# Performance work log

Hardware: AMD Instinct MI355X
Metric: run time of the kernel (lower is better)

The kernel has to match this reference:

```python
import jax, jax.numpy as jnp
import numpy as np

DIM = 8      # channels (from CxWxW_Attention(8, 4, False))
HEADS = 4    # num_heads
EPS = 1e-12  # torch F.normalize eps


def setup_inputs() -> dict:
    key = jax.random.key(0)
    k0, k1, k2, k3 = jax.random.split(key, 4)
    b, c, h, w = 16, DIM, 512, 512
    x = jax.random.normal(k0, (b, c, h, w), jnp.float32)
    # 1x1 conv producing qkv (bias=False): weight (3c, c)
    w_qkv = jax.random.normal(k1, (3 * c, c), jnp.float32) * 0.1
    # 3x3 depthwise conv on qkv, groups=3c: weight (3c, 1, 3, 3)
    w_dw = jax.random.normal(k2, (3 * c, 1, 3, 3), jnp.float32) * 0.1
    # 1x1 projection out: weight (c, c)
    w_out = jax.random.normal(k3, (c, c), jnp.float32) * 0.1
    # per-head learned temperature, init ones; broadcasts over (b, head, c, w, w)
    temperature = jnp.ones((HEADS, 1, 1, 1), jnp.float32)
    return dict(x=x, w_qkv=w_qkv, w_dw=w_dw, w_out=w_out, temperature=temperature)


def _dwconv3x3(x, wgt):
    # depthwise 3x3, padding=1, groups = channels
    C = x.shape[1]
    return jax.lax.conv_general_dilated(
        x, wgt, window_strides=(1, 1), padding=((1, 1), (1, 1)),
        dimension_numbers=("NCHW", "OIHW", "NCHW"), feature_group_count=C)


def _l2norm(t):
    # torch.nn.functional.normalize along last dim
    n = jnp.sqrt(jnp.sum(t * t, axis=-1, keepdims=True))
    return t / jnp.maximum(n, EPS)


def reference(x, w_qkv, w_dw, w_out, temperature):
    b, c, h, w = x.shape
    heads, ch = HEADS, c // HEADS
    # qkv = dwconv3x3(conv1x1(x))
    qkv = jnp.einsum("bchw,oc->bohw", x, w_qkv)
    qkv = _dwconv3x3(qkv, w_dw)
    q, k, v = jnp.split(qkv, 3, axis=1)
    # rearrange 'b (head ch) h w -> b head ch w h' : width attends, height = feature
    def split_heads(t):
        return t.reshape(b, heads, ch, h, w).transpose(0, 1, 2, 4, 3)
    q, k, v = split_heads(q), split_heads(k), split_heads(v)
    q = _l2norm(q)
    k = _l2norm(k)
    # attention map of shape (b, head, ch, W, W)  -> the 'C x W x W' attention
    attn = jnp.einsum("bncwh,bncvh->bncwv", q, k) * temperature
    attn = jax.nn.softmax(attn, axis=-1)
    out = jnp.einsum("bncwv,bncvh->bncwh", attn, v)  # (b, head, ch, w, h)
    # rearrange back 'b head ch w h -> b (head ch) h w'
    out = out.transpose(0, 1, 2, 4, 3).reshape(b, c, h, w)
    return jnp.einsum("bchw,oc->bohw", out, w_out)
```

## Files before the change

kernel.cpp:

```cpp
#include <hip/hip_runtime.h>
#include <hip/hip_bf16.h>

typedef __attribute__((ext_vector_type(4))) float f32x4;
typedef __attribute__((ext_vector_type(2))) float f32x2;
typedef __attribute__((ext_vector_type(8))) short s16x8;
typedef __attribute__((ext_vector_type(4))) short s16x4;
typedef __attribute__((ext_vector_type(4))) unsigned short u16x4;

#define HW 512
#define NSLICE 128

union B4 { s16x4 v; __hip_bfloat16 e[4]; };

__global__ __launch_bounds__(256) void qkv_fused(
    const float* __restrict__ x, const float* __restrict__ wqkv,
    const float* __restrict__ wdw,
    __hip_bfloat16* __restrict__ qT, __hip_bfloat16* __restrict__ kT,
    __hip_bfloat16* __restrict__ vS,
    float* __restrict__ qss, float* __restrict__ kss)
{
  const int b = blockIdx.y;
  const int tile = blockIdx.x;
  const int h0 = (tile >> 4) * 32;
  const int w0 = (tile & 15) * 32;
  const int tid = threadIdx.x;

  __shared__ float ts[4][1156][2];
  __shared__ float colsq[4][8][32];
  __shared__ float wq_s[24][8];
  __shared__ float wd_s[24][12];

  if (tid < 192) wq_s[tid >> 3][tid & 7] = wqkv[tid];
  if (tid < 216) wd_s[tid / 9][tid % 9] = wdw[tid];

  float xr[5][8];
  #pragma unroll
  for (int p = 0; p < 5; ++p) {
    int i = tid + p * 256;
    if (i < 1156) {
      int ih = h0 - 1 + i / 34, iw = w0 - 1 + i % 34;
      bool ok = (ih >= 0 && ih < HW && iw >= 0 && iw < HW);
      #pragma unroll
      for (int c = 0; c < 8; ++c)
        xr[p][c] = ok ? x[((size_t)(b * 8 + c) * HW + ih) * HW + iw] : 0.f;
    }
  }
  __syncthreads();

  const int tw = tid & 31;
  const int th = tid >> 5;
  const int lane = tid & 63;
  const int wv = tid >> 6;

  #pragma unroll
  for (int g = 0; g < 3; ++g) {
    #pragma unroll
    for (int p = 0; p < 5; ++p) {
      int i = tid + p * 256;
      if (i < 1156) {
        #pragma unroll
        for (int op = 0; op < 4; ++op) {
          const int o = g * 8 + op * 2;
          float a0 = 0.f, a1 = 0.f;
          #pragma unroll
          for (int c = 0; c < 8; ++c) {
            a0 += xr[p][c] * wq_s[o][c];
            a1 += xr[p][c] * wq_s[o + 1][c];
          }
          ts[op][i][0] = a0;
          ts[op][i][1] = a1;
        }
      }
    }
    __syncthreads();

    #pragma unroll
    for (int op = 0; op < 4; ++op) {
      const int o = g * 8 + op * 2;
      float w2[6][3][2];
      #pragma unroll
      for (int r = 0; r < 6; ++r)
        #pragma unroll
        for (int c = 0; c < 3; ++c) {
          f32x2 v = *(const f32x2*)&ts[op][(4 * th + r) * 34 + tw + c][0];
          w2[r][c][0] = v[0];
          w2[r][c][1] = v[1];
        }
      float o0[4], o1[4];
      #pragma unroll
      for (int r = 0; r < 4; ++r) { o0[r] = 0.f; o1[r] = 0.f; }
      #pragma unroll
      for (int di = 0; di < 3; ++di)
        #pragma unroll
        for (int dj = 0; dj < 3; ++dj) {
          const float wd0 = wd_s[o][di * 3 + dj];
          const float wd1 = wd_s[o + 1][di * 3 + dj];
          #pragma unroll
          for (int r = 0; r < 4; ++r) {
            o0[r] += w2[r + di][dj][0] * wd0;
            o1[r] += w2[r + di][dj][1] * wd1;
          }
        }
      if (g < 2) {
        float s0 = o0[0]*o0[0] + o0[1]*o0[1] + o0[2]*o0[2] + o0[3]*o0[3];
        float s1 = o1[0]*o1[0] + o1[1]*o1[1] + o1[2]*o1[2] + o1[3]*o1[3];
        s0 += __shfl_xor(s0, 32);
        s1 += __shfl_xor(s1, 32);
        if (lane < 32) {
          colsq[wv][op * 2][tw] = s0;
          colsq[wv][op * 2 + 1][tw] = s1;
        }
        B4 u0, u1;
        #pragma unroll
        for (int r = 0; r < 4; ++r) {
          u0.e[r] = __float2bfloat16(o0[r]);
          u1.e[r] = __float2bfloat16(o1[r]);
        }
        __hip_bfloat16* base = (g == 0) ? qT : kT;
        size_t a0i = (size_t)(b * 8 + op * 2) * HW * HW
                   + (size_t)(h0 >> 5) * HW * 32 + (size_t)(w0 + tw) * 32 + 4 * th;
        *(s16x4*)(base + a0i) = u0.v;
        *(s16x4*)(base + a0i + (size_t)HW * HW) = u1.v;
      } else {
        __hip_bfloat16* vb0 = vS + (size_t)(b * 8 + op * 2) * HW * HW
                            + (size_t)(w0 >> 5) * HW * 32 + (size_t)(h0 + 4 * th) * 32 + tw;
        __hip_bfloat16* vb1 = vb0 + (size_t)HW * HW;
        #pragma unroll
        for (int r = 0; r < 4; ++r) {
          vb0[r * 32] = __float2bfloat16(o0[r]);
          vb1[r * 32] = __float2bfloat16(o1[r]);
        }
      }
    }
    __syncthreads();

    if (g < 2) {
      const int o = tid >> 5, w = tid & 31;
      float s = colsq[0][o][w] + colsq[1][o][w] + colsq[2][o][w] + colsq[3][o][w];
      float* dst = (g == 0 ? qss : kss) + (size_t)(b * 8 + o) * HW + w0 + w;
      atomicAdd(dst, s);
    }
  }
}

#define QROW 1040
#define LDS_QP   0
#define OFF_RMAX 66560
#define OFF_RSUM 68608
#define OFF_RMAXF 70656
#define OFF_RSINV 70912
#define OFF_SQ   71168
#define OFF_SK   71424
#define ATTN_LDS_SIZE 73472

#define GL4(D, VOFF, BASE) \
  asm volatile("global_load_dwordx4 %0, %1, %2 offset:0"    : "=v"(D[0]) : "v"(VOFF), "s"(BASE)); \
  asm volatile("global_load_dwordx4 %0, %1, %2 offset:1024" : "=v"(D[1]) : "v"(VOFF), "s"(BASE)); \
  asm volatile("global_load_dwordx4 %0, %1, %2 offset:2048" : "=v"(D[2]) : "v"(VOFF), "s"(BASE)); \
  asm volatile("global_load_dwordx4 %0, %1, %2 offset:3072" : "=v"(D[3]) : "v"(VOFF), "s"(BASE));

#define LOADSETK(BF, CHN) { \
  const char* bk_ = ks + (size_t)(CHN) * 32768; \
  GL4(BF, voffK, bk_) }

#define LOADSETV(VF, CHN) { \
  const char* bv_ = vs + (size_t)(CHN) * 32768; \
  GL4(VF, voffK, bv_) }

#define WAITV(N) \
  asm volatile("s_waitcnt vmcnt(" #N ")"); \
  __builtin_amdgcn_sched_barrier(0);

#define LDSQ(QF, S) { \
    const int cq_ = (S) * 64 + klo; \
    _Pragma("unroll") for (int m_ = 0; m_ < 4; ++m_) \
      QF[m_] = *(const s16x8*)(ldsQ + (m_ * 16 + arow) * QROW + cq_); }

#define LOADP(AF, S) { \
    const int cbp_ = (S) * 64 + klo; \
    _Pragma("unroll") for (int m_ = 0; m_ < 4; ++m_) { \
      const int row_ = m_ * 16 + arow; \
      AF[m_] = *(const s16x8*)(ldsP + row_ * 1024 + (cbp_ ^ ((row_ & 7) << 4))); } }
#define MFMA16(AF, BF, ACC) { \
    _Pragma("unroll") for (int m_ = 0; m_ < 4; ++m_) \
      _Pragma("unroll") for (int n_ = 0; n_ < 4; ++n_) \
        ACC[m_][n_] = __builtin_amdgcn_mfma_f32_16x16x32_bf16(AF[m_], BF[n_], ACC[m_][n_], 0, 0, 0); }

__global__ __launch_bounds__(512, 1) void attn_kernel(
    const __hip_bfloat16* __restrict__ qT, const __hip_bfloat16* __restrict__ kT,
    const __hip_bfloat16* __restrict__ vS, __hip_bfloat16* __restrict__ Obuf,
    const float* __restrict__ qss, const float* __restrict__ kss,
    const float* __restrict__ temp)
{
  extern __shared__ char smem[];
  char* ldsQ = smem + LDS_QP;
  char* ldsP = smem + LDS_QP;
  float* red_max  = (float*)(smem + OFF_RMAX);
  float* red_sum  = (float*)(smem + OFF_RSUM);
  float* red_maxf = (float*)(smem + OFF_RMAXF);
  float* rsinv    = (float*)(smem + OFF_RSINV);
  float* sq_l     = (float*)(smem + OFF_SQ);
  float* sk_l     = (float*)(smem + OFF_SK);

  const int tid = threadIdx.x;
  const int lane = tid & 63;
  const int wv = tid >> 6;
  const int p = blockIdx.x;
  const int slice = (p & 7) + 8 * (p >> 6);
  const int rblk = (p >> 3) & 7;
  const int w0 = rblk * 64;
  const size_t sbase = (size_t)slice * HW * HW;
  const char* qs = (const char*)(qT + sbase);
  const char* ks = (const char*)(kT + sbase);
  const char* vs = (const char*)(vS + sbase);

  const int klo = (lane >> 4) << 4;
  const int arow = lane & 15;
  const int voffK = (wv * 64 + arow) * 64 + klo;

  {
    const int r = tid >> 3;
    const int seg = tid & 7;
    #pragma unroll
    for (int i = 0; i < 8; ++i) {
      const int chn_i = seg * 2 + (i >> 2);
      s16x8 v = *(const s16x8*)(qs + (size_t)chn_i * 32768 + (size_t)(w0 + r) * 64 + (i & 3) * 16);
      *(s16x8*)(ldsQ + r * QROW + seg * 128 + i * 16) = v;
    }
  }
  const float tmp = temp[(slice & 7) >> 1];
  if (tid < 64) sq_l[tid] = tmp / fmaxf(sqrtf(qss[(size_t)slice * HW + w0 + tid]), 1e-12f);
  sk_l[tid] = 1.f / fmaxf(sqrtf(kss[(size_t)slice * HW + tid]), 1e-12f);
  __syncthreads();

  f32x4 acc[4][4];
  #pragma unroll
  for (int m = 0; m < 4; ++m)
    #pragma unroll
    for (int n = 0; n < 4; ++n) acc[m][n] = (f32x4){0.f, 0.f, 0.f, 0.f};
  __builtin_amdgcn_sched_barrier(0);

  s16x8 bfA[4], bfB[4], bfC[4], bfD[4];
  LOADSETK(bfA, 0)
  LOADSETK(bfB, 1)
  LOADSETK(bfC, 2)
  LOADSETK(bfD, 3)

  #pragma unroll
  for (int g = 0; g < 3; ++g) {
    { s16x8 qf[4]; LDSQ(qf, 4 * g + 0) WAITV(12) MFMA16(qf, bfA, acc) } LOADSETK(bfA, 4 * g + 4)
    { s16x8 qf[4]; LDSQ(qf, 4 * g + 1) WAITV(12) MFMA16(qf, bfB, acc) } LOADSETK(bfB, 4 * g + 5)
    { s16x8 qf[4]; LDSQ(qf, 4 * g + 2) WAITV(12) MFMA16(qf, bfC, acc) } LOADSETK(bfC, 4 * g + 6)
    { s16x8 qf[4]; LDSQ(qf, 4 * g + 3) WAITV(12) MFMA16(qf, bfD, acc) } LOADSETK(bfD, 4 * g + 7)
  }
  { s16x8 qf[4]; LDSQ(qf, 12) WAITV(12) MFMA16(qf, bfA, acc) }
  { s16x8 qf[4]; LDSQ(qf, 13) WAITV(8)  MFMA16(qf, bfB, acc) }
  { s16x8 qf[4]; LDSQ(qf, 14) WAITV(4)  MFMA16(qf, bfC, acc) }
  { s16x8 qf[4]; LDSQ(qf, 15) WAITV(0)  MFMA16(qf, bfD, acc) }
  __syncthreads();

  float srow[4][4], scol[4];
  #pragma unroll
  for (int m = 0; m < 4; ++m)
    #pragma unroll
    for (int r = 0; r < 4; ++r)
      srow[m][r] = sq_l[m * 16 + ((lane >> 4) << 2) + r];
  #pragma unroll
  for (int n = 0; n < 4; ++n) scol[n] = sk_l[wv * 64 + n * 16 + (lane & 15)];

  float rmax[4][4];
  #pragma unroll
  for (int m = 0; m < 4; ++m)
    #pragma unroll
    for (int r = 0; r < 4; ++r) {
      float mx = -1e30f;
      #pragma unroll
      for (int n = 0; n < 4; ++n) {
        float v = acc[m][n][r] * srow[m][r] * scol[n];
        acc[m][n][r] = v;
        mx = fmaxf(mx, v);
      }
      mx = fmaxf(mx, __shfl_xor(mx, 1));
      mx = fmaxf(mx, __shfl_xor(mx, 2));
      mx = fmaxf(mx, __shfl_xor(mx, 4));
      mx = fmaxf(mx, __shfl_xor(mx, 8));
      rmax[m][r] = mx;
    }
  if ((lane & 15) == 0) {
    #pragma unroll
    for (int m = 0; m < 4; ++m)
      #pragma unroll
      for (int r = 0; r < 4; ++r)
        red_max[(m * 16 + ((lane >> 4) << 2) + r) * 8 + wv] = rmax[m][r];
  }
  __syncthreads();
  if (tid < 64) {
    float mx = red_max[tid * 8];
    #pragma unroll
    for (int g = 1; g < 8; ++g) mx = fmaxf(mx, red_max[tid * 8 + g]);
    red_maxf[tid] = mx;
  }
  __syncthreads();

  float gmax[4][4];
  #pragma unroll
  for (int m = 0; m < 4; ++m)
    #pragma unroll
    for (int r = 0; r < 4; ++r)
      gmax[m][r] = red_maxf[m * 16 + ((lane >> 4) << 2) + r];

  s16x8 vfA[4], vfB[4], vfC[4], vfD[4];
  LOADSETV(vfA, 0)
  LOADSETV(vfB, 1)
  LOADSETV(vfC, 2)
  LOADSETV(vfD, 3)

  float rs[4][4];
  #pragma unroll
  for (int m = 0; m < 4; ++m)
    #pragma unroll
    for (int r = 0; r < 4; ++r) rs[m][r] = 0.f;
  #pragma unroll
  for (int m = 0; m < 4; ++m)
    #pragma unroll
    for (int n = 0; n < 4; ++n)
      #pragma unroll
      for (int r = 0; r < 4; ++r) {
        int row = m * 16 + ((lane >> 4) << 2) + r;
        int col = wv * 64 + n * 16 + (lane & 15);
        float pv = __expf(acc[m][n][r] - gmax[m][r]);
        rs[m][r] += pv;
        *(__hip_bfloat16*)(ldsP + row * 1024 + ((col * 2) ^ ((row & 7) << 4))) =
            __float2bfloat16(pv);
      }
  #pragma unroll
  for (int m = 0; m < 4; ++m)
    #pragma unroll
    for (int r = 0; r < 4; ++r) {
      float s = rs[m][r];
      s += __shfl_xor(s, 1);
      s += __shfl_xor(s, 2);
      s += __shfl_xor(s, 4);
      s += __shfl_xor(s, 8);
      if ((lane & 15) == 0)
        red_sum[(m * 16 + ((lane >> 4) << 2) + r) * 8 + wv] = s;
    }
  __syncthreads();
  if (tid < 64) {
    float s = 0.f;
    #pragma unroll
    for (int g = 0; g < 8; ++g) s += red_sum[tid * 8 + g];
    rsinv[tid] = 1.f / s;
  }

  f32x4 acc2[4][4];
  #pragma unroll
  for (int m = 0; m < 4; ++m)
    #pragma unroll
    for (int n = 0; n < 4; ++n) acc2[m][n] = (f32x4){0.f, 0.f, 0.f, 0.f};

  #pragma unroll
  for (int g = 0; g < 3; ++g) {
    { s16x8 pf[4]; LOADP(pf, 4 * g + 0) WAITV(12) MFMA16(pf, vfA, acc2) } LOADSETV(vfA, 4 * g + 4)
    { s16x8 pf[4]; LOADP(pf, 4 * g + 1) WAITV(12) MFMA16(pf, vfB, acc2) } LOADSETV(vfB, 4 * g + 5)
    { s16x8 pf[4]; LOADP(pf, 4 * g + 2) WAITV(12) MFMA16(pf, vfC, acc2) } LOADSETV(vfC, 4 * g + 6)
    { s16x8 pf[4]; LOADP(pf, 4 * g + 3) WAITV(12) MFMA16(pf, vfD, acc2) } LOADSETV(vfD, 4 * g + 7)
  }
  { s16x8 pf[4]; LOADP(pf, 12) WAITV(12) MFMA16(pf, vfA, acc2) }
  { s16x8 pf[4]; LOADP(pf, 13) WAITV(8)  MFMA16(pf, vfB, acc2) }
  { s16x8 pf[4]; LOADP(pf, 14) WAITV(4)  MFMA16(pf, vfC, acc2) }
  { s16x8 pf[4]; LOADP(pf, 15) WAITV(0)  MFMA16(pf, vfD, acc2) }
  __syncthreads();

  float rinv[4][4];
  #pragma unroll
  for (int m = 0; m < 4; ++m)
    #pragma unroll
    for (int r = 0; r < 4; ++r)
      rinv[m][r] = rsinv[m * 16 + ((lane >> 4) << 2) + r];

  char* ldsO = ldsP + wv * 8192;
  #pragma unroll
  for (int m = 0; m < 4; ++m)
    #pragma unroll
    for (int n = 0; n < 4; ++n)
      #pragma unroll
      for (int r = 0; r < 4; ++r) {
        int row = m * 16 + ((lane >> 4) << 2) + r;
        int col = n * 16 + (lane & 15);
        *(__hip_bfloat16*)(ldsO + row * 128 + col * 2) =
            __float2bfloat16(acc2[m][n][r] * rinv[m][r]);
      }
  __syncthreads();
  __hip_bfloat16* ob = Obuf + sbase + (size_t)w0 * HW + wv * 64;
  #pragma unroll
  for (int it = 0; it < 8; ++it) {
    int row = it * 8 + (lane >> 3);
    int c = (lane & 7) << 4;
    s16x8 v = *(const s16x8*)(ldsO + row * 128 + c);
    *(s16x8*)((char*)ob + (size_t)row * 1024 + c) = v;
  }
}

__global__ __launch_bounds__(256) void proj_kernel(
    const __hip_bfloat16* __restrict__ Obuf, const float* __restrict__ wout,
    float* __restrict__ out)
{
  const int b = blockIdx.y;
  const int t = blockIdx.x;
  const int h0 = (t >> 5) * 64;
  const int w0 = (t & 31) * 16;
  const int tid = threadIdx.x;
  __shared__ float os[8][16][65];
  __shared__ float wo_s[64];
  if (tid < 64) wo_s[tid] = wout[tid];
  {
    int r = tid >> 4;
    int c4 = (tid & 15) * 4;
    #pragma unroll
    for (int o = 0; o < 8; ++o) {
      const __hip_bfloat16* p = Obuf + ((size_t)(b * 8 + o) * HW + w0 + r) * HW + h0 + c4;
      u16x4 v = *(const u16x4*)p;
      #pragma unroll
      for (int i = 0; i < 4; ++i)
        os[o][r][c4 + i] = __uint_as_float((unsigned)v[i] << 16);
    }
  }
  __syncthreads();
  const int w = tid & 15;
  #pragma unroll
  for (int ih = 0; ih < 4; ++ih) {
    int h = ih * 16 + (tid >> 4);
    float ov[8];
    #pragma unroll
    for (int o = 0; o < 8; ++o) ov[o] = os[o][w][h];
    #pragma unroll
    for (int jo = 0; jo < 8; ++jo) {
      float a = 0.f;
      #pragma unroll
      for (int o = 0; o < 8; ++o) a += ov[o] * wo_s[jo * 8 + o];
      out[((size_t)(b * 8 + jo) * HW + h0 + h) * HW + w0 + w] = a;
    }
  }
}

extern "C" void kernel_launch(void* const* d_in, const int* in_sizes, int n_in,
                              void* d_out, int out_size, void* d_ws, size_t ws_size,
                              hipStream_t stream) {
  (void)in_sizes; (void)n_in; (void)out_size; (void)ws_size;
  const float* x    = (const float*)d_in[0];
  const float* wqkv = (const float*)d_in[1];
  const float* wdw  = (const float*)d_in[2];
  const float* wout = (const float*)d_in[3];
  const float* temp = (const float*)d_in[4];
  float* out = (float*)d_out;

  char* ws = (char*)d_ws;
  const size_t plane = (size_t)NSLICE * HW * HW * 2;
  __hip_bfloat16* qT = (__hip_bfloat16*)(ws);
  __hip_bfloat16* kT = (__hip_bfloat16*)(ws + plane);
  __hip_bfloat16* vS = (__hip_bfloat16*)(ws + 2 * plane);
  __hip_bfloat16* Ob = (__hip_bfloat16*)(ws + 3 * plane);
  float* qss = (float*)(ws + 4 * plane);
  float* kss = (float*)(ws + 4 * plane + (size_t)NSLICE * HW * 4);

  hipMemsetAsync(qss, 0, 2 * (size_t)NSLICE * HW * 4, stream);
  qkv_fused<<<dim3(256, 16), 256, 0, stream>>>(x, wqkv, wdw, qT, kT, vS, qss, kss);
  hipFuncSetAttribute((const void*)attn_kernel,
                      hipFuncAttributeMaxDynamicSharedMemorySize, ATTN_LDS_SIZE);
  attn_kernel<<<dim3(1024), 512, ATTN_LDS_SIZE, stream>>>(qT, kT, vS, Ob, qss, kss, temp);
  proj_kernel<<<dim3(256, 16), 256, 0, stream>>>(Ob, wout, out);
}
```

Baseline: 312.5 us.

## Swizzle Q LDS layout, halve prefetch depth, raise attention occupancy target

```diff
diff --git a/kernel.cpp b/kernel.cpp
--- a/kernel.cpp
+++ b/kernel.cpp
@@ -143,15 +143,14 @@
   }
 }
 
-#define QROW 1040
 #define LDS_QP   0
-#define OFF_RMAX 66560
-#define OFF_RSUM 68608
-#define OFF_RMAXF 70656
-#define OFF_RSINV 70912
-#define OFF_SQ   71168
-#define OFF_SK   71424
-#define ATTN_LDS_SIZE 73472
+#define OFF_RMAX 65536
+#define OFF_RSUM 67584
+#define OFF_RMAXF 69632
+#define OFF_RSINV 69888
+#define OFF_SQ   70144
+#define OFF_SK   70400
+#define ATTN_LDS_SIZE 72448
 
 #define GL4(D, VOFF, BASE) \
   asm volatile("global_load_dwordx4 %0, %1, %2 offset:0"    : "=v"(D[0]) : "v"(VOFF), "s"(BASE)); \
@@ -171,22 +170,18 @@
   asm volatile("s_waitcnt vmcnt(" #N ")"); \
   __builtin_amdgcn_sched_barrier(0);
 
-#define LDSQ(QF, S) { \
-    const int cq_ = (S) * 64 + klo; \
-    _Pragma("unroll") for (int m_ = 0; m_ < 4; ++m_) \
-      QF[m_] = *(const s16x8*)(ldsQ + (m_ * 16 + arow) * QROW + cq_); }
-
-#define LOADP(AF, S) { \
-    const int cbp_ = (S) * 64 + klo; \
+#define LDSQP(QF, S) { \
+    const int c_ = (S) * 64 + klo; \
     _Pragma("unroll") for (int m_ = 0; m_ < 4; ++m_) { \
       const int row_ = m_ * 16 + arow; \
-      AF[m_] = *(const s16x8*)(ldsP + row_ * 1024 + (cbp_ ^ ((row_ & 7) << 4))); } }
+      QF[m_] = *(const s16x8*)(ldsQ + row_ * 1024 + (c_ ^ ((row_ & 7) << 4))); } }
+
 #define MFMA16(AF, BF, ACC) { \
     _Pragma("unroll") for (int m_ = 0; m_ < 4; ++m_) \
       _Pragma("unroll") for (int n_ = 0; n_ < 4; ++n_) \
         ACC[m_][n_] = __builtin_amdgcn_mfma_f32_16x16x32_bf16(AF[m_], BF[n_], ACC[m_][n_], 0, 0, 0); }
 
-__global__ __launch_bounds__(512, 1) void attn_kernel(
+__global__ __launch_bounds__(512, 4) void attn_kernel(
     const __hip_bfloat16* __restrict__ qT, const __hip_bfloat16* __restrict__ kT,
     const __hip_bfloat16* __restrict__ vS, __hip_bfloat16* __restrict__ Obuf,
     const float* __restrict__ qss, const float* __restrict__ kss,
@@ -224,8 +219,9 @@
     #pragma unroll
     for (int i = 0; i < 8; ++i) {
       const int chn_i = seg * 2 + (i >> 2);
+      const int col = seg * 128 + i * 16;
       s16x8 v = *(const s16x8*)(qs + (size_t)chn_i * 32768 + (size_t)(w0 + r) * 64 + (i & 3) * 16);
-      *(s16x8*)(ldsQ + r * QROW + seg * 128 + i * 16) = v;
+      *(s16x8*)(ldsQ + r * 1024 + (col ^ ((r & 7) << 4))) = v;
     }
   }
   const float tmp = temp[(slice & 7) >> 1];
@@ -240,23 +236,17 @@
     for (int n = 0; n < 4; ++n) acc[m][n] = (f32x4){0.f, 0.f, 0.f, 0.f};
   __builtin_amdgcn_sched_barrier(0);
 
-  s16x8 bfA[4], bfB[4], bfC[4], bfD[4];
+  s16x8 bfA[4], bfB[4];
   LOADSETK(bfA, 0)
   LOADSETK(bfB, 1)
-  LOADSETK(bfC, 2)
-  LOADSETK(bfD, 3)
-
-  #pragma unroll
-  for (int g = 0; g < 3; ++g) {
-    { s16x8 qf[4]; LDSQ(qf, 4 * g + 0) WAITV(12) MFMA16(qf, bfA, acc) } LOADSETK(bfA, 4 * g + 4)
-    { s16x8 qf[4]; LDSQ(qf, 4 * g + 1) WAITV(12) MFMA16(qf, bfB, acc) } LOADSETK(bfB, 4 * g + 5)
-    { s16x8 qf[4]; LDSQ(qf, 4 * g + 2) WAITV(12) MFMA16(qf, bfC, acc) } LOADSETK(bfC, 4 * g + 6)
-    { s16x8 qf[4]; LDSQ(qf, 4 * g + 3) WAITV(12) MFMA16(qf, bfD, acc) } LOADSETK(bfD, 4 * g + 7)
-  }
-  { s16x8 qf[4]; LDSQ(qf, 12) WAITV(12) MFMA16(qf, bfA, acc) }
-  { s16x8 qf[4]; LDSQ(qf, 13) WAITV(8)  MFMA16(qf, bfB, acc) }
-  { s16x8 qf[4]; LDSQ(qf, 14) WAITV(4)  MFMA16(qf, bfC, acc) }
-  { s16x8 qf[4]; LDSQ(qf, 15) WAITV(0)  MFMA16(qf, bfD, acc) }
+
+  #pragma unroll
+  for (int g = 0; g < 7; ++g) {
+    { s16x8 qf[4]; LDSQP(qf, 2 * g + 0) WAITV(4) MFMA16(qf, bfA, acc) } LOADSETK(bfA, 2 * g + 2)
+    { s16x8 qf[4]; LDSQP(qf, 2 * g + 1) WAITV(4) MFMA16(qf, bfB, acc) } LOADSETK(bfB, 2 * g + 3)
+  }
+  { s16x8 qf[4]; LDSQP(qf, 14) WAITV(4) MFMA16(qf, bfA, acc) }
+  { s16x8 qf[4]; LDSQP(qf, 15) WAITV(0) MFMA16(qf, bfB, acc) }
   __syncthreads();
 
   float srow[4][4], scol[4];
@@ -309,11 +299,9 @@
     for (int r = 0; r < 4; ++r)
       gmax[m][r] = red_maxf[m * 16 + ((lane >> 4) << 2) + r];
 
-  s16x8 vfA[4], vfB[4], vfC[4], vfD[4];
+  s16x8 vfA[4], vfB[4];
   LOADSETV(vfA, 0)
   LOADSETV(vfB, 1)
-  LOADSETV(vfC, 2)
-  LOADSETV(vfD, 3)
 
   float rs[4][4];
   #pragma unroll
@@ -360,16 +348,12 @@
     for (int n = 0; n < 4; ++n) acc2[m][n] = (f32x4){0.f, 0.f, 0.f, 0.f};
 
   #pragma unroll
-  for (int g = 0; g < 3; ++g) {
-    { s16x8 pf[4]; LOADP(pf, 4 * g + 0) WAITV(12) MFMA16(pf, vfA, acc2) } LOADSETV(vfA, 4 * g + 4)
-    { s16x8 pf[4]; LOADP(pf, 4 * g + 1) WAITV(12) MFMA16(pf, vfB, acc2) } LOADSETV(vfB, 4 * g + 5)
-    { s16x8 pf[4]; LOADP(pf, 4 * g + 2) WAITV(12) MFMA16(pf, vfC, acc2) } LOADSETV(vfC, 4 * g + 6)
-    { s16x8 pf[4]; LOADP(pf, 4 * g + 3) WAITV(12) MFMA16(pf, vfD, acc2) } LOADSETV(vfD, 4 * g + 7)
-  }
-  { s16x8 pf[4]; LOADP(pf, 12) WAITV(12) MFMA16(pf, vfA, acc2) }
-  { s16x8 pf[4]; LOADP(pf, 13) WAITV(8)  MFMA16(pf, vfB, acc2) }
-  { s16x8 pf[4]; LOADP(pf, 14) WAITV(4)  MFMA16(pf, vfC, acc2) }
-  { s16x8 pf[4]; LOADP(pf, 15) WAITV(0)  MFMA16(pf, vfD, acc2) }
+  for (int g = 0; g < 7; ++g) {
+    { s16x8 pf[4]; LDSQP(pf, 2 * g + 0) WAITV(4) MFMA16(pf, vfA, acc2) } LOADSETV(vfA, 2 * g + 2)
+    { s16x8 pf[4]; LDSQP(pf, 2 * g + 1) WAITV(4) MFMA16(pf, vfB, acc2) } LOADSETV(vfB, 2 * g + 3)
+  }
+  { s16x8 pf[4]; LDSQP(pf, 14) WAITV(4) MFMA16(pf, vfA, acc2) }
+  { s16x8 pf[4]; LDSQP(pf, 15) WAITV(0) MFMA16(pf, vfB, acc2) }
   __syncthreads();
 
   float rinv[4][4];
```

Result: slower. 329.4 us (+5.4%).

## Split attention block across 16 waves with 32 key columns each

Applied to the files above, without the earlier changes.

```diff
diff --git a/kernel.cpp b/kernel.cpp
--- a/kernel.cpp
+++ b/kernel.cpp
@@ -146,26 +146,24 @@
 #define QROW 1040
 #define LDS_QP   0
 #define OFF_RMAX 66560
-#define OFF_RSUM 68608
-#define OFF_RMAXF 70656
-#define OFF_RSINV 70912
-#define OFF_SQ   71168
-#define OFF_SK   71424
-#define ATTN_LDS_SIZE 73472
-
-#define GL4(D, VOFF, BASE) \
+#define OFF_RSUM 70656
+#define OFF_RMAXF 74752
+#define OFF_RSINV 75008
+#define OFF_SQ   75264
+#define OFF_SK   75520
+#define ATTN_LDS_SIZE 77568
+
+#define GL2(D, VOFF, BASE) \
   asm volatile("global_load_dwordx4 %0, %1, %2 offset:0"    : "=v"(D[0]) : "v"(VOFF), "s"(BASE)); \
-  asm volatile("global_load_dwordx4 %0, %1, %2 offset:1024" : "=v"(D[1]) : "v"(VOFF), "s"(BASE)); \
-  asm volatile("global_load_dwordx4 %0, %1, %2 offset:2048" : "=v"(D[2]) : "v"(VOFF), "s"(BASE)); \
-  asm volatile("global_load_dwordx4 %0, %1, %2 offset:3072" : "=v"(D[3]) : "v"(VOFF), "s"(BASE));
+  asm volatile("global_load_dwordx4 %0, %1, %2 offset:1024" : "=v"(D[1]) : "v"(VOFF), "s"(BASE));
 
 #define LOADSETK(BF, CHN) { \
   const char* bk_ = ks + (size_t)(CHN) * 32768; \
-  GL4(BF, voffK, bk_) }
+  GL2(BF, voffK, bk_) }
 
 #define LOADSETV(VF, CHN) { \
   const char* bv_ = vs + (size_t)(CHN) * 32768; \
-  GL4(VF, voffK, bv_) }
+  GL2(VF, voffK, bv_) }
 
 #define WAITV(N) \
   asm volatile("s_waitcnt vmcnt(" #N ")"); \
@@ -181,12 +179,13 @@
     _Pragma("unroll") for (int m_ = 0; m_ < 4; ++m_) { \
       const int row_ = m_ * 16 + arow; \
       AF[m_] = *(const s16x8*)(ldsP + row_ * 1024 + (cbp_ ^ ((row_ & 7) << 4))); } }
-#define MFMA16(AF, BF, ACC) { \
+
+#define MFMA8(AF, BF, ACC) { \
     _Pragma("unroll") for (int m_ = 0; m_ < 4; ++m_) \
-      _Pragma("unroll") for (int n_ = 0; n_ < 4; ++n_) \
+      _Pragma("unroll") for (int n_ = 0; n_ < 2; ++n_) \
         ACC[m_][n_] = __builtin_amdgcn_mfma_f32_16x16x32_bf16(AF[m_], BF[n_], ACC[m_][n_], 0, 0, 0); }
 
-__global__ __launch_bounds__(512, 1) void attn_kernel(
+__global__ __launch_bounds__(1024, 4) void attn_kernel(
     const __hip_bfloat16* __restrict__ qT, const __hip_bfloat16* __restrict__ kT,
     const __hip_bfloat16* __restrict__ vS, __hip_bfloat16* __restrict__ Obuf,
     const float* __restrict__ qss, const float* __restrict__ kss,
@@ -216,31 +215,30 @@
 
   const int klo = (lane >> 4) << 4;
   const int arow = lane & 15;
-  const int voffK = (wv * 64 + arow) * 64 + klo;
+  const int voffK = (wv * 32 + arow) * 64 + klo;
 
   {
-    const int r = tid >> 3;
-    const int seg = tid & 7;
-    #pragma unroll
-    for (int i = 0; i < 8; ++i) {
-      const int chn_i = seg * 2 + (i >> 2);
-      s16x8 v = *(const s16x8*)(qs + (size_t)chn_i * 32768 + (size_t)(w0 + r) * 64 + (i & 3) * 16);
-      *(s16x8*)(ldsQ + r * QROW + seg * 128 + i * 16) = v;
-    }
+    const int r = tid >> 4;
+    const int seg = tid & 15;
+    const char* src = qs + (size_t)seg * 32768 + (size_t)(w0 + r) * 64;
+    char* dst = ldsQ + r * QROW + seg * 64;
+    #pragma unroll
+    for (int i = 0; i < 4; ++i)
+      *(s16x8*)(dst + i * 16) = *(const s16x8*)(src + i * 16);
   }
   const float tmp = temp[(slice & 7) >> 1];
   if (tid < 64) sq_l[tid] = tmp / fmaxf(sqrtf(qss[(size_t)slice * HW + w0 + tid]), 1e-12f);
-  sk_l[tid] = 1.f / fmaxf(sqrtf(kss[(size_t)slice * HW + tid]), 1e-12f);
-  __syncthreads();
-
-  f32x4 acc[4][4];
-  #pragma unroll
-  for (int m = 0; m < 4; ++m)
-    #pragma unroll
-    for (int n = 0; n < 4; ++n) acc[m][n] = (f32x4){0.f, 0.f, 0.f, 0.f};
+  if (tid < 512) sk_l[tid] = 1.f / fmaxf(sqrtf(kss[(size_t)slice * HW + tid]), 1e-12f);
+  __syncthreads();
+
+  f32x4 acc[4][2];
+  #pragma unroll
+  for (int m = 0; m < 4; ++m)
+    #pragma unroll
+    for (int n = 0; n < 2; ++n) acc[m][n] = (f32x4){0.f, 0.f, 0.f, 0.f};
   __builtin_amdgcn_sched_barrier(0);
 
-  s16x8 bfA[4], bfB[4], bfC[4], bfD[4];
+  s16x8 bfA[2], bfB[2], bfC[2], bfD[2];
   LOADSETK(bfA, 0)
   LOADSETK(bfB, 1)
   LOADSETK(bfC, 2)
@@ -248,25 +246,25 @@
 
   #pragma unroll
   for (int g = 0; g < 3; ++g) {
-    { s16x8 qf[4]; LDSQ(qf, 4 * g + 0) WAITV(12) MFMA16(qf, bfA, acc) } LOADSETK(bfA, 4 * g + 4)
-    { s16x8 qf[4]; LDSQ(qf, 4 * g + 1) WAITV(12) MFMA16(qf, bfB, acc) } LOADSETK(bfB, 4 * g + 5)
-    { s16x8 qf[4]; LDSQ(qf, 4 * g + 2) WAITV(12) MFMA16(qf, bfC, acc) } LOADSETK(bfC, 4 * g + 6)
-    { s16x8 qf[4]; LDSQ(qf, 4 * g + 3) WAITV(12) MFMA16(qf, bfD, acc) } LOADSETK(bfD, 4 * g + 7)
-  }
-  { s16x8 qf[4]; LDSQ(qf, 12) WAITV(12) MFMA16(qf, bfA, acc) }
-  { s16x8 qf[4]; LDSQ(qf, 13) WAITV(8)  MFMA16(qf, bfB, acc) }
-  { s16x8 qf[4]; LDSQ(qf, 14) WAITV(4)  MFMA16(qf, bfC, acc) }
-  { s16x8 qf[4]; LDSQ(qf, 15) WAITV(0)  MFMA16(qf, bfD, acc) }
-  __syncthreads();
-
-  float srow[4][4], scol[4];
+    { s16x8 qf[4]; LDSQ(qf, 4 * g + 0) WAITV(6) MFMA8(qf, bfA, acc) } LOADSETK(bfA, 4 * g + 4)
+    { s16x8 qf[4]; LDSQ(qf, 4 * g + 1) WAITV(6) MFMA8(qf, bfB, acc) } LOADSETK(bfB, 4 * g + 5)
+    { s16x8 qf[4]; LDSQ(qf, 4 * g + 2) WAITV(6) MFMA8(qf, bfC, acc) } LOADSETK(bfC, 4 * g + 6)
+    { s16x8 qf[4]; LDSQ(qf, 4 * g + 3) WAITV(6) MFMA8(qf, bfD, acc) } LOADSETK(bfD, 4 * g + 7)
+  }
+  { s16x8 qf[4]; LDSQ(qf, 12) WAITV(6) MFMA8(qf, bfA, acc) }
+  { s16x8 qf[4]; LDSQ(qf, 13) WAITV(4) MFMA8(qf, bfB, acc) }
+  { s16x8 qf[4]; LDSQ(qf, 14) WAITV(2) MFMA8(qf, bfC, acc) }
+  { s16x8 qf[4]; LDSQ(qf, 15) WAITV(0) MFMA8(qf, bfD, acc) }
+  __syncthreads();
+
+  float srow[4][4], scol[2];
   #pragma unroll
   for (int m = 0; m < 4; ++m)
     #pragma unroll
     for (int r = 0; r < 4; ++r)
       srow[m][r] = sq_l[m * 16 + ((lane >> 4) << 2) + r];
   #pragma unroll
-  for (int n = 0; n < 4; ++n) scol[n] = sk_l[wv * 64 + n * 16 + (lane & 15)];
+  for (int n = 0; n < 2; ++n) scol[n] = sk_l[wv * 32 + n * 16 + (lane & 15)];
 
   float rmax[4][4];
   #pragma unroll
@@ -275,7 +273,7 @@
     for (int r = 0; r < 4; ++r) {
       float mx = -1e30f;
       #pragma unroll
-      for (int n = 0; n < 4; ++n) {
+      for (int n = 0; n < 2; ++n) {
         float v = acc[m][n][r] * srow[m][r] * scol[n];
         acc[m][n][r] = v;
         mx = fmaxf(mx, v);
@@ -291,13 +289,13 @@
     for (int m = 0; m < 4; ++m)
       #pragma unroll
       for (int r = 0; r < 4; ++r)
-        red_max[(m * 16 + ((lane >> 4) << 2) + r) * 8 + wv] = rmax[m][r];
+        red_max[(m * 16 + ((lane >> 4) << 2) + r) * 16 + wv] = rmax[m][r];
   }
   __syncthreads();
   if (tid < 64) {
-    float mx = red_max[tid * 8];
-    #pragma unroll
-    for (int g = 1; g < 8; ++g) mx = fmaxf(mx, red_max[tid * 8 + g]);
+    float mx = red_max[tid * 16];
+    #pragma unroll
+    for (int g = 1; g < 16; ++g) mx = fmaxf(mx, red_max[tid * 16 + g]);
     red_maxf[tid] = mx;
   }
   __syncthreads();
@@ -309,7 +307,7 @@
     for (int r = 0; r < 4; ++r)
       gmax[m][r] = red_maxf[m * 16 + ((lane >> 4) << 2) + r];
 
-  s16x8 vfA[4], vfB[4], vfC[4], vfD[4];
+  s16x8 vfA[2], vfB[2], vfC[2], vfD[2];
   LOADSETV(vfA, 0)
   LOADSETV(vfB, 1)
   LOADSETV(vfC, 2)
@@ -323,11 +321,11 @@
   #pragma unroll
   for (int m = 0; m < 4; ++m)
     #pragma unroll
-    for (int n = 0; n < 4; ++n)
+    for (int n = 0; n < 2; ++n)
       #pragma unroll
       for (int r = 0; r < 4; ++r) {
         int row = m * 16 + ((lane >> 4) << 2) + r;
-        int col = wv * 64 + n * 16 + (lane & 15);
+        int col = wv * 32 + n * 16 + (lane & 15);
         float pv = __expf(acc[m][n][r] - gmax[m][r]);
         rs[m][r] += pv;
         *(__hip_bfloat16*)(ldsP + row * 1024 + ((col * 2) ^ ((row & 7) << 4))) =
@@ -343,33 +341,33 @@
       s += __shfl_xor(s, 4);
       s += __shfl_xor(s, 8);
       if ((lane & 15) == 0)
-        red_sum[(m * 16 + ((lane >> 4) << 2) + r) * 8 + wv] = s;
+        red_sum[(m * 16 + ((lane >> 4) << 2) + r) * 16 + wv] = s;
     }
   __syncthreads();
   if (tid < 64) {
     float s = 0.f;
     #pragma unroll
-    for (int g = 0; g < 8; ++g) s += red_sum[tid * 8 + g];
+    for (int g = 0; g < 16; ++g) s += red_sum[tid * 16 + g];
     rsinv[tid] = 1.f / s;
   }
 
-  f32x4 acc2[4][4];
-  #pragma unroll
-  for (int m = 0; m < 4; ++m)
-    #pragma unroll
-    for (int n = 0; n < 4; ++n) acc2[m][n] = (f32x4){0.f, 0.f, 0.f, 0.f};
+  f32x4 acc2[4][2];
+  #pragma unroll
+  for (int m = 0; m < 4; ++m)
+    #pragma unroll
+    for (int n = 0; n < 2; ++n) acc2[m][n] = (f32x4){0.f, 0.f, 0.f, 0.f};
 
   #pragma unroll
   for (int g = 0; g < 3; ++g) {
-    { s16x8 pf[4]; LOADP(pf, 4 * g + 0) WAITV(12) MFMA16(pf, vfA, acc2) } LOADSETV(vfA, 4 * g + 4)
-    { s16x8 pf[4]; LOADP(pf, 4 * g + 1) WAITV(12) MFMA16(pf, vfB, acc2) } LOADSETV(vfB, 4 * g + 5)
-    { s16x8 pf[4]; LOADP(pf, 4 * g + 2) WAITV(12) MFMA16(pf, vfC, acc2) } LOADSETV(vfC, 4 * g + 6)
-    { s16x8 pf[4]; LOADP(pf, 4 * g + 3) WAITV(12) MFMA16(pf, vfD, acc2) } LOADSETV(vfD, 4 * g + 7)
-  }
-  { s16x8 pf[4]; LOADP(pf, 12) WAITV(12) MFMA16(pf, vfA, acc2) }
-  { s16x8 pf[4]; LOADP(pf, 13) WAITV(8)  MFMA16(pf, vfB, acc2) }
-  { s16x8 pf[4]; LOADP(pf, 14) WAITV(4)  MFMA16(pf, vfC, acc2) }
-  { s16x8 pf[4]; LOADP(pf, 15) WAITV(0)  MFMA16(pf, vfD, acc2) }
+    { s16x8 pf[4]; LOADP(pf, 4 * g + 0) WAITV(6) MFMA8(pf, vfA, acc2) } LOADSETV(vfA, 4 * g + 4)
+    { s16x8 pf[4]; LOADP(pf, 4 * g + 1) WAITV(6) MFMA8(pf, vfB, acc2) } LOADSETV(vfB, 4 * g + 5)
+    { s16x8 pf[4]; LOADP(pf, 4 * g + 2) WAITV(6) MFMA8(pf, vfC, acc2) } LOADSETV(vfC, 4 * g + 6)
+    { s16x8 pf[4]; LOADP(pf, 4 * g + 3) WAITV(6) MFMA8(pf, vfD, acc2) } LOADSETV(vfD, 4 * g + 7)
+  }
+  { s16x8 pf[4]; LOADP(pf, 12) WAITV(6) MFMA8(pf, vfA, acc2) }
+  { s16x8 pf[4]; LOADP(pf, 13) WAITV(4) MFMA8(pf, vfB, acc2) }
+  { s16x8 pf[4]; LOADP(pf, 14) WAITV(2) MFMA8(pf, vfC, acc2) }
+  { s16x8 pf[4]; LOADP(pf, 15) WAITV(0) MFMA8(pf, vfD, acc2) }
   __syncthreads();
 
   float rinv[4][4];
@@ -379,26 +377,26 @@
     for (int r = 0; r < 4; ++r)
       rinv[m][r] = rsinv[m * 16 + ((lane >> 4) << 2) + r];
 
-  char* ldsO = ldsP + wv * 8192;
-  #pragma unroll
-  for (int m = 0; m < 4; ++m)
-    #pragma unroll
-    for (int n = 0; n < 4; ++n)
+  #pragma unroll
+  for (int m = 0; m < 4; ++m)
+    #pragma unroll
+    for (int n = 0; n < 2; ++n)
       #pragma unroll
       for (int r = 0; r < 4; ++r) {
         int row = m * 16 + ((lane >> 4) << 2) + r;
-        int col = n * 16 + (lane & 15);
-        *(__hip_bfloat16*)(ldsO + row * 128 + col * 2) =
+        int col = wv * 32 + n * 16 + (lane & 15);
+        *(__hip_bfloat16*)(ldsP + row * 1024 + col * 2) =
             __float2bfloat16(acc2[m][n][r] * rinv[m][r]);
       }
   __syncthreads();
-  __hip_bfloat16* ob = Obuf + sbase + (size_t)w0 * HW + wv * 64;
-  #pragma unroll
-  for (int it = 0; it < 8; ++it) {
-    int row = it * 8 + (lane >> 3);
-    int c = (lane & 7) << 4;
-    s16x8 v = *(const s16x8*)(ldsO + row * 128 + c);
-    *(s16x8*)((char*)ob + (size_t)row * 1024 + c) = v;
+  {
+    const int row = tid >> 4;
+    const int seg = tid & 15;
+    const char* src = ldsP + row * 1024 + seg * 64;
+    char* dst = (char*)(Obuf + sbase + (size_t)w0 * HW) + (size_t)row * 1024 + seg * 64;
+    #pragma unroll
+    for (int i = 0; i < 4; ++i)
+      *(s16x8*)(dst + i * 16) = *(const s16x8*)(src + i * 16);
   }
 }
 
@@ -468,6 +466,6 @@
   qkv_fused<<<dim3(256, 16), 256, 0, stream>>>(x, wqkv, wdw, qT, kT, vS, qss, kss);
   hipFuncSetAttribute((const void*)attn_kernel,
                       hipFuncAttributeMaxDynamicSharedMemorySize, ATTN_LDS_SIZE);
-  attn_kernel<<<dim3(1024), 512, ATTN_LDS_SIZE, stream>>>(qT, kT, vS, Ob, qss, kss, temp);
+  attn_kernel<<<dim3(1024), 1024, ATTN_LDS_SIZE, stream>>>(qT, kT, vS, Ob, qss, kss, temp);
   proj_kernel<<<dim3(256, 16), 256, 0, stream>>>(Ob, wout, out);
 }
```

New measurement: 327.9 us. 1.05x slower.
